# Performance work log

Measured on AMD Instinct MI355X. Metric: run time of the kernel, lower is better.

## Reference

```python
import jax, jax.numpy as jnp
import numpy as np

NUM_NODES_GLOBAL = 100000
EMBED_DIM = 256
NUM_RELATIONS = 16
N_LOCAL = 16384
N_EDGES = 131072
N_QUERIES = 4096


def setup_inputs() -> dict:
    key = jax.random.key(0)
    ks = jax.random.split(key, 12)
    node_emb = jax.random.normal(ks[0], (NUM_NODES_GLOBAL, EMBED_DIM), dtype=jnp.float32)
    # RGCN layer 1 params: per-relation weight (R, in, out), root weight, bias
    w1 = jax.random.normal(ks[1], (NUM_RELATIONS, EMBED_DIM, EMBED_DIM), dtype=jnp.float32) * 0.05
    root1 = jax.random.normal(ks[2], (EMBED_DIM, EMBED_DIM), dtype=jnp.float32) * 0.05
    b1 = jnp.zeros((EMBED_DIM,), dtype=jnp.float32)
    w2 = jax.random.normal(ks[3], (NUM_RELATIONS, EMBED_DIM, EMBED_DIM), dtype=jnp.float32) * 0.05
    root2 = jax.random.normal(ks[4], (EMBED_DIM, EMBED_DIM), dtype=jnp.float32) * 0.05
    b2 = jnp.zeros((EMBED_DIM,), dtype=jnp.float32)
    edge_index = jax.random.randint(ks[5], (2, N_EDGES), 0, N_LOCAL, dtype=jnp.int64)
    edge_type = jax.random.randint(ks[6], (N_EDGES,), 0, NUM_RELATIONS, dtype=jnp.int64)
    entity_ids = jax.random.randint(ks[7], (N_LOCAL,), 0, NUM_NODES_GLOBAL, dtype=jnp.int64)
    batch_ids = jnp.sort(jax.random.randint(ks[8], (N_LOCAL,), 0, N_QUERIES, dtype=jnp.int64))
    return {"node_emb": node_emb, "w1": w1, "root1": root1, "b1": b1,
            "w2": w2, "root2": root2, "b2": b2,
            "edge_index": edge_index, "edge_type": edge_type,
            "entity_ids": entity_ids, "batch_ids": batch_ids}


def rgcn_layer(x, W, Wroot, b, src, tgt, edge_type, num_relations):
    """PyG RGCNConv (num_bases=None, aggr='mean', root_weight=True, bias=True).

    out[i] = sum_r mean_{j: (j -r-> i)} x_j @ W[r]  +  x_i @ Wroot + b
    Aggregation done per (target, relation) bucket, then a single (N,R,d)x(R,d,d) einsum.
    """
    n = x.shape[0]
    d = x.shape[1]
    bucket = tgt * num_relations + edge_type  # (E,) combined (node, relation) key
    ones = jnp.ones(src.shape, dtype=x.dtype)
    cnt = jax.ops.segment_sum(ones, bucket, num_segments=n * num_relations)
    agg = jax.ops.segment_sum(x[src], bucket, num_segments=n * num_relations)
    agg = agg.reshape(n, num_relations, d) / jnp.maximum(cnt, 1.0).reshape(n, num_relations, 1)
    return jnp.einsum('nrd,rdo->no', agg, W) + x @ Wroot + b


def reference(node_emb, w1, root1, b1, w2, root2, b2, edge_index, edge_type, entity_ids, batch_ids):
    x = node_emb[entity_ids]                      # (N_local, d) gather from global table
    src, tgt = edge_index[0], edge_index[1]
    x = rgcn_layer(x, w1, root1, b1, src, tgt, edge_type, NUM_RELATIONS)
    x = rgcn_layer(x, w2, root2, b2, src, tgt, edge_type, NUM_RELATIONS)
    # scatter-sum readout per query
    return jax.ops.segment_sum(x, batch_ids, num_segments=N_QUERIES)
```

## Files before the change

kernel.cpp:

```cpp
#include <hip/hip_runtime.h>
#include <hip/hip_bf16.h>

#define NLOCAL 16384
#define NEDGES 131072
#define NREL   16
#define DIM    256
#define NQ     4096
#define NBLKS  512

typedef __bf16 bf16x8 __attribute__((ext_vector_type(8)));
typedef float  f32x4  __attribute__((ext_vector_type(4)));
typedef unsigned short u16x8 __attribute__((ext_vector_type(8)));

static __device__ __forceinline__ unsigned short f2bf(float f) {
    union { float f; unsigned u; } v; v.f = f;
    unsigned r = v.u + 0x7FFFu + ((v.u >> 16) & 1u);
    return (unsigned short)(r >> 16);
}
static __device__ __forceinline__ float bf2f(unsigned short s) {
    union { unsigned u; float f; } v; v.u = ((unsigned)s) << 16;
    return v.f;
}

__global__ void k_gather(const float* __restrict__ emb, const int* __restrict__ ids,
                         unsigned short* __restrict__ x0) {
    int gid = blockIdx.x * blockDim.x + threadIdx.x;
    int i = gid >> 5, c8 = gid & 31;
    int e = ids[i];
    const f32x4* src = (const f32x4*)(emb + (size_t)e * DIM + c8 * 8);
    f32x4 a = src[0], b = src[1];
    u16x8 u;
    u[0] = f2bf(a[0]); u[1] = f2bf(a[1]); u[2] = f2bf(a[2]); u[3] = f2bf(a[3]);
    u[4] = f2bf(b[0]); u[5] = f2bf(b[1]); u[6] = f2bf(b[2]); u[7] = f2bf(b[3]);
    *(u16x8*)&x0[(size_t)i * DIM + c8 * 8] = u;
}

__global__ void k_transpose_all(const float* __restrict__ w1, const float* __restrict__ r1,
                                const float* __restrict__ w2, const float* __restrict__ r2,
                                unsigned short* __restrict__ WT1, unsigned short* __restrict__ rT1,
                                unsigned short* __restrict__ WT2, unsigned short* __restrict__ rT2) {
    __shared__ float t[64][65];
    int blk = blockIdx.x;
    const float* W; unsigned short* WT; int tr;
    if (blk < 256)      { W = w1 + (size_t)(blk >> 4) * DIM * DIM; WT = WT1 + (size_t)(blk >> 4) * DIM * DIM; tr = blk & 15; }
    else if (blk < 272) { W = r1; WT = rT1; tr = blk - 256; }
    else if (blk < 528) { int q = blk - 272; W = w2 + (size_t)(q >> 4) * DIM * DIM; WT = WT2 + (size_t)(q >> 4) * DIM * DIM; tr = q & 15; }
    else                { W = r2; WT = rT2; tr = blk - 528; }
    int tk = (tr >> 2) << 6;
    int to = (tr & 3) << 6;
    #pragma unroll
    for (int it = 0; it < 16; ++it) {
        int el = it * 256 + threadIdx.x;
        int row = el >> 6, col = el & 63;
        t[row][col] = W[(size_t)(tk + row) * DIM + to + col];
    }
    __syncthreads();
    #pragma unroll
    for (int it = 0; it < 16; ++it) {
        int el = it * 256 + threadIdx.x;
        int row = el >> 6, col = el & 63;
        WT[(size_t)(to + row) * DIM + tk + col] = f2bf(t[col][row]);
    }
}

__global__ void k_hist2(const int* __restrict__ eidx, const int* __restrict__ etype,
                        unsigned int* __restrict__ cnt, int* __restrict__ bh) {
    __shared__ int h[NREL];
    int tid = threadIdx.x;
    if (tid < NREL) h[tid] = 0;
    __syncthreads();
    int e = blockIdx.x * 256 + tid;
    int rel = etype[e];
    int tgt = eidx[NEDGES + e];
    atomicAdd(&cnt[tgt * NREL + rel], 1u);
    atomicAdd(&h[rel], 1);
    __syncthreads();
    if (tid < NREL) bh[tid * NBLKS + blockIdx.x] = h[tid];
}

__global__ void k_scan_par(int* __restrict__ bh, int* __restrict__ meta) {
    __shared__ int tot[NREL];
    __shared__ int base[NREL];
    int w = threadIdx.x >> 6, lane = threadIdx.x & 63;
    int vals[8];
    int run = 0;
    #pragma unroll
    for (int c = 0; c < 8; ++c) {
        int v = bh[w * NBLKS + c * 64 + lane];
        int s = v;
        #pragma unroll
        for (int off = 1; off < 64; off <<= 1) {
            int t = __shfl_up(s, off);
            if (lane >= off) s += t;
        }
        vals[c] = run + s - v;
        run += __shfl(s, 63);
    }
    if (lane == 0) tot[w] = run;
    __syncthreads();
    if (threadIdx.x == 0) {
        int s = 0;
        for (int r = 0; r < NREL; ++r) { base[r] = s; meta[16 + r] = s; s += (tot[r] + 63) & ~63; }
        meta[32] = s;
    }
    __syncthreads();
    int b = base[w];
    #pragma unroll
    for (int c = 0; c < 8; ++c) bh[w * NBLKS + c * 64 + lane] = vals[c] + b;
}

__global__ void k_place2(const int* __restrict__ eidx, const int* __restrict__ etype,
                         const int* __restrict__ bh, int* __restrict__ ssrc,
                         int* __restrict__ stgt) {
    __shared__ int cur[NREL];
    int tid = threadIdx.x;
    if (tid < NREL) cur[tid] = bh[tid * NBLKS + blockIdx.x];
    __syncthreads();
    int e = blockIdx.x * 256 + tid;
    int rel = etype[e];
    int pos = atomicAdd(&cur[rel], 1);
    ssrc[pos] = eidx[e];
    stgt[pos] = eidx[NEDGES + e];
}

#define AS_IDX(row, c16) ((row) * 64 + (((c16) ^ ((row) & 7)) << 3))

__launch_bounds__(256)
__global__ void k_gemm_root(const unsigned short* __restrict__ X, const unsigned short* __restrict__ BT,
                            const float* __restrict__ bias, unsigned short* __restrict__ Y) {
    __shared__ __align__(16) unsigned short As[64 * 64];
    __shared__ __align__(16) unsigned short Bs[256 * 64];
    int tid = threadIdx.x;
    int wave = tid >> 6, lane = tid & 63;
    int l16 = lane & 15, grp = lane >> 4;
    int bm = blockIdx.x;

    f32x4 acc[4][4];
    #pragma unroll
    for (int i = 0; i < 4; ++i)
        #pragma unroll
        for (int j = 0; j < 4; ++j) acc[i][j] = f32x4{0.f, 0.f, 0.f, 0.f};

    int arow = tid >> 3, ac16 = tid & 7;
    for (int kt = 0; kt < 4; ++kt) {
        #pragma unroll
        for (int it = 0; it < 2; ++it) {
            int row = it * 32 + arow;
            u16x8 u = *(const u16x8*)&X[(size_t)(bm * 64 + row) * DIM + kt * 64 + ac16 * 8];
            *(u16x8*)&As[AS_IDX(row, ac16)] = u;
        }
        #pragma unroll
        for (int it = 0; it < 8; ++it) {
            int flat = it * 256 + tid;
            int row = flat >> 3, c16 = flat & 7;
            u16x8 u = *(const u16x8*)&BT[(size_t)row * DIM + kt * 64 + c16 * 8];
            *(u16x8*)&Bs[AS_IDX(row, c16)] = u;
        }
        __syncthreads();
        #pragma unroll
        for (int kk = 0; kk < 2; ++kk) {
            bf16x8 a[4], b[4];
            #pragma unroll
            for (int i = 0; i < 4; ++i) {
                int row = i * 16 + l16;
                a[i] = *(const bf16x8*)&As[AS_IDX(row, kk * 4 + grp)];
            }
            #pragma unroll
            for (int j = 0; j < 4; ++j) {
                int row = wave * 64 + j * 16 + l16;
                b[j] = *(const bf16x8*)&Bs[AS_IDX(row, kk * 4 + grp)];
            }
            #pragma unroll
            for (int i = 0; i < 4; ++i)
                #pragma unroll
                for (int j = 0; j < 4; ++j)
                    acc[i][j] = __builtin_amdgcn_mfma_f32_16x16x32_bf16(a[i], b[j], acc[i][j], 0, 0, 0);
        }
        __syncthreads();
    }
    #pragma unroll
    for (int i = 0; i < 4; ++i)
        #pragma unroll
        for (int reg = 0; reg < 4; ++reg) {
            int row = i * 16 + grp * 4 + reg;
            int gr = bm * 64 + row;
            #pragma unroll
            for (int j = 0; j < 4; ++j) {
                int col = wave * 64 + j * 16 + l16;
                float v = acc[i][j][reg] + bias[col];
                float vo = __shfl_xor(v, 1);
                if (!(lane & 1)) {
                    unsigned pk = (unsigned)f2bf(v) | ((unsigned)f2bf(vo) << 16);
                    *(unsigned*)&Y[(size_t)gr * DIM + col] = pk;
                }
            }
        }
}

__launch_bounds__(256)
__global__ void k_gemm_edge(const unsigned short* __restrict__ X, const unsigned short* __restrict__ WT,
                            const int* __restrict__ ssrc, const int* __restrict__ stgt,
                            const unsigned int* __restrict__ cnt, const int* __restrict__ meta,
                            unsigned short* __restrict__ Y) {
    int base = blockIdx.x * 64;
    if (base >= meta[32]) return;
    int rel = 0;
    while (rel < 15 && meta[16 + rel + 1] <= base) ++rel;
    const unsigned short* BT = WT + (size_t)rel * DIM * DIM;

    __shared__ __align__(16) unsigned short As[64 * 64];
    __shared__ __align__(16) unsigned short Bs[256 * 64];
    int tid = threadIdx.x;
    int wave = tid >> 6, lane = tid & 63;
    int l16 = lane & 15, grp = lane >> 4;

    f32x4 acc[4][4];
    #pragma unroll
    for (int i = 0; i < 4; ++i)
        #pragma unroll
        for (int j = 0; j < 4; ++j) acc[i][j] = f32x4{0.f, 0.f, 0.f, 0.f};

    int arow = tid >> 3, ac16 = tid & 7;
    int s0 = ssrc[base + arow];
    int s1 = ssrc[base + 32 + arow];
    for (int kt = 0; kt < 4; ++kt) {
        #pragma unroll
        for (int it = 0; it < 2; ++it) {
            int row = it * 32 + arow;
            int s = it ? s1 : s0;
            u16x8 u = {};
            if (s >= 0) u = *(const u16x8*)&X[(size_t)s * DIM + kt * 64 + ac16 * 8];
            *(u16x8*)&As[AS_IDX(row, ac16)] = u;
        }
        #pragma unroll
        for (int it = 0; it < 8; ++it) {
            int flat = it * 256 + tid;
            int row = flat >> 3, c16 = flat & 7;
            u16x8 u = *(const u16x8*)&BT[(size_t)row * DIM + kt * 64 + c16 * 8];
            *(u16x8*)&Bs[AS_IDX(row, c16)] = u;
        }
        __syncthreads();
        #pragma unroll
        for (int kk = 0; kk < 2; ++kk) {
            bf16x8 a[4], b[4];
            #pragma unroll
            for (int i = 0; i < 4; ++i) {
                int row = i * 16 + l16;
                a[i] = *(const bf16x8*)&As[AS_IDX(row, kk * 4 + grp)];
            }
            #pragma unroll
            for (int j = 0; j < 4; ++j) {
                int row = wave * 64 + j * 16 + l16;
                b[j] = *(const bf16x8*)&Bs[AS_IDX(row, kk * 4 + grp)];
            }
            #pragma unroll
            for (int i = 0; i < 4; ++i)
                #pragma unroll
                for (int j = 0; j < 4; ++j)
                    acc[i][j] = __builtin_amdgcn_mfma_f32_16x16x32_bf16(a[i], b[j], acc[i][j], 0, 0, 0);
        }
        __syncthreads();
    }
    #pragma unroll
    for (int i = 0; i < 4; ++i)
        #pragma unroll
        for (int reg = 0; reg < 4; ++reg) {
            int row = i * 16 + grp * 4 + reg;
            int e = base + row;
            int s = ssrc[e];
            if (s < 0) continue;
            int tgt = stgt[e];
            float rc = 1.0f / fmaxf((float)cnt[tgt * NREL + rel], 1.0f);
            unsigned short* Yrow = Y + (size_t)tgt * DIM;
            #pragma unroll
            for (int j = 0; j < 4; ++j) {
                int col = wave * 64 + j * 16 + l16;
                float v = acc[i][j][reg] * rc;
                float vo = __shfl_xor(v, 1);
                if (!(lane & 1)) {
                    __hip_bfloat162 hv;
                    ((unsigned short*)&hv)[0] = f2bf(v);
                    ((unsigned short*)&hv)[1] = f2bf(vo);
                    unsafeAtomicAdd((__hip_bfloat162*)(Yrow + col), hv);
                }
            }
        }
}

__global__ void k_readout(const unsigned short* __restrict__ X2, const int* __restrict__ bids,
                          float* __restrict__ out) {
    int gid = blockIdx.x * blockDim.x + threadIdx.x;
    int g = gid >> 5, c8 = gid & 31;
    int i0 = g * 8;
    float a[8];
    #pragma unroll
    for (int j = 0; j < 8; ++j) a[j] = 0.f;
    int curq = bids[i0];
    #pragma unroll
    for (int t = 0; t < 8; ++t) {
        int i = i0 + t;
        int q = bids[i];
        if (q != curq) {
            #pragma unroll
            for (int j = 0; j < 8; ++j) {
                unsafeAtomicAdd(&out[(size_t)curq * DIM + c8 * 8 + j], a[j]);
                a[j] = 0.f;
            }
            curq = q;
        }
        u16x8 v = *(const u16x8*)&X2[(size_t)i * DIM + c8 * 8];
        #pragma unroll
        for (int j = 0; j < 8; ++j) a[j] += bf2f(v[j]);
    }
    #pragma unroll
    for (int j = 0; j < 8; ++j)
        unsafeAtomicAdd(&out[(size_t)curq * DIM + c8 * 8 + j], a[j]);
}

extern "C" void kernel_launch(void* const* d_in, const int* in_sizes, int n_in,
                              void* d_out, int out_size, void* d_ws, size_t ws_size,
                              hipStream_t stream) {
    const float* emb   = (const float*)d_in[0];
    const float* w1    = (const float*)d_in[1];
    const float* root1 = (const float*)d_in[2];
    const float* b1    = (const float*)d_in[3];
    const float* w2    = (const float*)d_in[4];
    const float* root2 = (const float*)d_in[5];
    const float* b2    = (const float*)d_in[6];
    const int* eidx    = (const int*)d_in[7];
    const int* etype   = (const int*)d_in[8];
    const int* eids    = (const int*)d_in[9];
    const int* bids    = (const int*)d_in[10];
    float* out = (float*)d_out;

    char* ws = (char*)d_ws;
    unsigned short* x0  = (unsigned short*)(ws + (size_t)(0 << 20));
    unsigned short* x1  = (unsigned short*)(ws + (size_t)(8 << 20));
    unsigned short* x2  = (unsigned short*)(ws + (size_t)(16 << 20));
    unsigned short* WT1 = (unsigned short*)(ws + (size_t)(24 << 20));
    unsigned short* rT1 = (unsigned short*)(ws + (size_t)(26 << 20));
    unsigned short* WT2 = (unsigned short*)(ws + (size_t)(27 << 20));
    unsigned short* rT2 = (unsigned short*)(ws + (size_t)(29 << 20));
    unsigned int*   cnt = (unsigned int*)(ws + (size_t)(30 << 20));
    int*           meta = (int*)(ws + (size_t)(31 << 20));
    int*           ssrc = (int*)(ws + (size_t)(31 << 20) + 4096);
    int*           stgt = (int*)(ws + (size_t)(32 << 20));
    int*           bh   = (int*)(ws + (size_t)(33 << 20));

    const int NBLK_EDGE = (NEDGES + NREL * 64) / 64;

    hipMemsetAsync(cnt, 0, (size_t)NLOCAL * NREL * 4, stream);
    hipMemsetAsync(ssrc, 0xFF, (size_t)(NEDGES + NREL * 64) * 4, stream);
    hipMemsetAsync(out, 0, (size_t)NQ * DIM * 4, stream);

    k_gather<<<2048, 256, 0, stream>>>(emb, eids, x0);
    k_transpose_all<<<544, 256, 0, stream>>>(w1, root1, w2, root2, WT1, rT1, WT2, rT2);
    k_hist2<<<NBLKS, 256, 0, stream>>>(eidx, etype, cnt, bh);
    k_scan_par<<<1, 1024, 0, stream>>>(bh, meta);
    k_place2<<<NBLKS, 256, 0, stream>>>(eidx, etype, bh, ssrc, stgt);

    k_gemm_root<<<NLOCAL / 64, 256, 0, stream>>>(x0, rT1, b1, x1);
    k_gemm_edge<<<NBLK_EDGE, 256, 0, stream>>>(x0, WT1, ssrc, stgt, cnt, meta, x1);
    k_gemm_root<<<NLOCAL / 64, 256, 0, stream>>>(x1, rT2, b2, x2);
    k_gemm_edge<<<NBLK_EDGE, 256, 0, stream>>>(x1, WT2, ssrc, stgt, cnt, meta, x2);

    k_readout<<<256, 256, 0, stream>>>(x2, bids, out);
}
```

Before: 505.6 us.

## Replace bf16 atomic scatter with per-edge buffer and CSR gather-combine

The edge GEMM now writes each scaled edge message to a per-slot buffer instead of doing bf16x2 atomic adds into the target rows. A per-target CSR (count, scan, placement) is built, and a new combine kernel sums the root output plus all incoming edge messages per target in fp32. The GEMMs also drop LDS staging of the weight tile, reading B fragments directly from global/L2, and double-buffer the A tile with one sync per k-step. This trades atomic contention and repeated bf16 rounding for extra memory traffic (a 64MB-class edge buffer written and re-read) plus two extra setup kernels.

```diff
diff --git a/kernel.cpp b/kernel.cpp
--- a/kernel.cpp
+++ b/kernel.cpp
@@ -7,9 +7,11 @@
 #define DIM    256
 #define NQ     4096
 #define NBLKS  512
+#define NSLOTS (NEDGES + NREL * 64)
 
 typedef __bf16 bf16x8 __attribute__((ext_vector_type(8)));
 typedef float  f32x4  __attribute__((ext_vector_type(4)));
+typedef unsigned short u16x4 __attribute__((ext_vector_type(4)));
 typedef unsigned short u16x8 __attribute__((ext_vector_type(8)));
 
 static __device__ __forceinline__ unsigned short f2bf(float f) {
@@ -64,7 +66,8 @@
 }
 
 __global__ void k_hist2(const int* __restrict__ eidx, const int* __restrict__ etype,
-                        unsigned int* __restrict__ cnt, int* __restrict__ bh) {
+                        unsigned int* __restrict__ cnt, unsigned int* __restrict__ cnt_t,
+                        int* __restrict__ bh) {
     __shared__ int h[NREL];
     int tid = threadIdx.x;
     if (tid < NREL) h[tid] = 0;
@@ -73,6 +76,7 @@
     int rel = etype[e];
     int tgt = eidx[NEDGES + e];
     atomicAdd(&cnt[tgt * NREL + rel], 1u);
+    atomicAdd(&cnt_t[tgt], 1u);
     atomicAdd(&h[rel], 1);
     __syncthreads();
     if (tid < NREL) bh[tid * NBLKS + blockIdx.x] = h[tid];
@@ -123,17 +127,57 @@
     stgt[pos] = eidx[NEDGES + e];
 }
 
+__global__ void k_scan_t(const unsigned int* __restrict__ cnt_t, int* __restrict__ row_ptr,
+                         int* __restrict__ cur) {
+    __shared__ int wsum[16];
+    int tid = threadIdx.x;
+    int wave = tid >> 6, lane = tid & 63;
+    int base = tid * 16;
+    int loc[16];
+    int s = 0;
+    #pragma unroll
+    for (int c = 0; c < 16; ++c) { loc[c] = s; s += (int)cnt_t[base + c]; }
+    int inc = s;
+    #pragma unroll
+    for (int off = 1; off < 64; off <<= 1) {
+        int t = __shfl_up(inc, off);
+        if (lane >= off) inc += t;
+    }
+    if (lane == 63) wsum[wave] = inc;
+    __syncthreads();
+    if (tid == 0) {
+        int a = 0;
+        for (int w = 0; w < 16; ++w) { int v = wsum[w]; wsum[w] = a; a += v; }
+    }
+    __syncthreads();
+    int excl = wsum[wave] + inc - s;
+    #pragma unroll
+    for (int c = 0; c < 16; ++c) { int v = excl + loc[c]; row_ptr[base + c] = v; cur[base + c] = v; }
+    if (tid == 1023) row_ptr[NLOCAL] = excl + s;
+}
+
+__global__ void k_place_t(const int* __restrict__ ssrc, const int* __restrict__ stgt,
+                          int* __restrict__ cur, int* __restrict__ elist) {
+    int p = blockIdx.x * 256 + threadIdx.x;
+    int s = ssrc[p];
+    if (s >= 0) {
+        int tgt = stgt[p];
+        int pos = atomicAdd(&cur[tgt], 1);
+        elist[pos] = p;
+    }
+}
+
 #define AS_IDX(row, c16) ((row) * 64 + (((c16) ^ ((row) & 7)) << 3))
 
 __launch_bounds__(256)
 __global__ void k_gemm_root(const unsigned short* __restrict__ X, const unsigned short* __restrict__ BT,
                             const float* __restrict__ bias, unsigned short* __restrict__ Y) {
-    __shared__ __align__(16) unsigned short As[64 * 64];
-    __shared__ __align__(16) unsigned short Bs[256 * 64];
+    __shared__ __align__(16) unsigned short As[2][64 * 64];
     int tid = threadIdx.x;
     int wave = tid >> 6, lane = tid & 63;
     int l16 = lane & 15, grp = lane >> 4;
     int bm = blockIdx.x;
+    int arow = tid >> 3, ac16 = tid & 7;
 
     f32x4 acc[4][4];
     #pragma unroll
@@ -141,42 +185,38 @@
         #pragma unroll
         for (int j = 0; j < 4; ++j) acc[i][j] = f32x4{0.f, 0.f, 0.f, 0.f};
 
-    int arow = tid >> 3, ac16 = tid & 7;
+    #pragma unroll
+    for (int it = 0; it < 2; ++it) {
+        int row = it * 32 + arow;
+        u16x8 u = *(const u16x8*)&X[(size_t)(bm * 64 + row) * DIM + ac16 * 8];
+        *(u16x8*)&As[0][AS_IDX(row, ac16)] = u;
+    }
     for (int kt = 0; kt < 4; ++kt) {
-        #pragma unroll
-        for (int it = 0; it < 2; ++it) {
-            int row = it * 32 + arow;
-            u16x8 u = *(const u16x8*)&X[(size_t)(bm * 64 + row) * DIM + kt * 64 + ac16 * 8];
-            *(u16x8*)&As[AS_IDX(row, ac16)] = u;
-        }
-        #pragma unroll
-        for (int it = 0; it < 8; ++it) {
-            int flat = it * 256 + tid;
-            int row = flat >> 3, c16 = flat & 7;
-            u16x8 u = *(const u16x8*)&BT[(size_t)row * DIM + kt * 64 + c16 * 8];
-            *(u16x8*)&Bs[AS_IDX(row, c16)] = u;
-        }
         __syncthreads();
+        if (kt < 3) {
+            #pragma unroll
+            for (int it = 0; it < 2; ++it) {
+                int row = it * 32 + arow;
+                u16x8 u = *(const u16x8*)&X[(size_t)(bm * 64 + row) * DIM + (kt + 1) * 64 + ac16 * 8];
+                *(u16x8*)&As[(kt + 1) & 1][AS_IDX(row, ac16)] = u;
+            }
+        }
+        const unsigned short* buf = As[kt & 1];
         #pragma unroll
         for (int kk = 0; kk < 2; ++kk) {
             bf16x8 a[4], b[4];
             #pragma unroll
-            for (int i = 0; i < 4; ++i) {
-                int row = i * 16 + l16;
-                a[i] = *(const bf16x8*)&As[AS_IDX(row, kk * 4 + grp)];
-            }
-            #pragma unroll
-            for (int j = 0; j < 4; ++j) {
-                int row = wave * 64 + j * 16 + l16;
-                b[j] = *(const bf16x8*)&Bs[AS_IDX(row, kk * 4 + grp)];
-            }
+            for (int i = 0; i < 4; ++i)
+                a[i] = *(const bf16x8*)&buf[AS_IDX(i * 16 + l16, kk * 4 + grp)];
+            #pragma unroll
+            for (int j = 0; j < 4; ++j)
+                b[j] = *(const bf16x8*)&BT[(size_t)(wave * 64 + j * 16 + l16) * DIM + kt * 64 + kk * 32 + grp * 8];
             #pragma unroll
             for (int i = 0; i < 4; ++i)
                 #pragma unroll
                 for (int j = 0; j < 4; ++j)
                     acc[i][j] = __builtin_amdgcn_mfma_f32_16x16x32_bf16(a[i], b[j], acc[i][j], 0, 0, 0);
         }
-        __syncthreads();
     }
     #pragma unroll
     for (int i = 0; i < 4; ++i)
@@ -201,18 +241,18 @@
 __global__ void k_gemm_edge(const unsigned short* __restrict__ X, const unsigned short* __restrict__ WT,
                             const int* __restrict__ ssrc, const int* __restrict__ stgt,
                             const unsigned int* __restrict__ cnt, const int* __restrict__ meta,
-                            unsigned short* __restrict__ Y) {
+                            unsigned short* __restrict__ ye) {
     int base = blockIdx.x * 64;
     if (base >= meta[32]) return;
     int rel = 0;
     while (rel < 15 && meta[16 + rel + 1] <= base) ++rel;
     const unsigned short* BT = WT + (size_t)rel * DIM * DIM;
 
-    __shared__ __align__(16) unsigned short As[64 * 64];
-    __shared__ __align__(16) unsigned short Bs[256 * 64];
+    __shared__ __align__(16) unsigned short As[2][64 * 64];
     int tid = threadIdx.x;
     int wave = tid >> 6, lane = tid & 63;
     int l16 = lane & 15, grp = lane >> 4;
+    int arow = tid >> 3, ac16 = tid & 7;
 
     f32x4 acc[4][4];
     #pragma unroll
@@ -220,46 +260,44 @@
         #pragma unroll
         for (int j = 0; j < 4; ++j) acc[i][j] = f32x4{0.f, 0.f, 0.f, 0.f};
 
-    int arow = tid >> 3, ac16 = tid & 7;
     int s0 = ssrc[base + arow];
     int s1 = ssrc[base + 32 + arow];
+    #pragma unroll
+    for (int it = 0; it < 2; ++it) {
+        int row = it * 32 + arow;
+        int s = it ? s1 : s0;
+        u16x8 u = {};
+        if (s >= 0) u = *(const u16x8*)&X[(size_t)s * DIM + ac16 * 8];
+        *(u16x8*)&As[0][AS_IDX(row, ac16)] = u;
+    }
     for (int kt = 0; kt < 4; ++kt) {
-        #pragma unroll
-        for (int it = 0; it < 2; ++it) {
-            int row = it * 32 + arow;
-            int s = it ? s1 : s0;
-            u16x8 u = {};
-            if (s >= 0) u = *(const u16x8*)&X[(size_t)s * DIM + kt * 64 + ac16 * 8];
-            *(u16x8*)&As[AS_IDX(row, ac16)] = u;
-        }
-        #pragma unroll
-        for (int it = 0; it < 8; ++it) {
-            int flat = it * 256 + tid;
-            int row = flat >> 3, c16 = flat & 7;
-            u16x8 u = *(const u16x8*)&BT[(size_t)row * DIM + kt * 64 + c16 * 8];
-            *(u16x8*)&Bs[AS_IDX(row, c16)] = u;
-        }
         __syncthreads();
+        if (kt < 3) {
+            #pragma unroll
+            for (int it = 0; it < 2; ++it) {
+                int row = it * 32 + arow;
+                int s = it ? s1 : s0;
+                u16x8 u = {};
+                if (s >= 0) u = *(const u16x8*)&X[(size_t)s * DIM + (kt + 1) * 64 + ac16 * 8];
+                *(u16x8*)&As[(kt + 1) & 1][AS_IDX(row, ac16)] = u;
+            }
+        }
+        const unsigned short* buf = As[kt & 1];
         #pragma unroll
         for (int kk = 0; kk < 2; ++kk) {
             bf16x8 a[4], b[4];
             #pragma unroll
-            for (int i = 0; i < 4; ++i) {
-                int row = i * 16 + l16;
-                a[i] = *(const bf16x8*)&As[AS_IDX(row, kk * 4 + grp)];
-            }
-            #pragma unroll
-            for (int j = 0; j < 4; ++j) {
-                int row = wave * 64 + j * 16 + l16;
-                b[j] = *(const bf16x8*)&Bs[AS_IDX(row, kk * 4 + grp)];
-            }
+            for (int i = 0; i < 4; ++i)
+                a[i] = *(const bf16x8*)&buf[AS_IDX(i * 16 + l16, kk * 4 + grp)];
+            #pragma unroll
+            for (int j = 0; j < 4; ++j)
+                b[j] = *(const bf16x8*)&BT[(size_t)(wave * 64 + j * 16 + l16) * DIM + kt * 64 + kk * 32 + grp * 8];
             #pragma unroll
             for (int i = 0; i < 4; ++i)
                 #pragma unroll
                 for (int j = 0; j < 4; ++j)
                     acc[i][j] = __builtin_amdgcn_mfma_f32_16x16x32_bf16(a[i], b[j], acc[i][j], 0, 0, 0);
         }
-        __syncthreads();
     }
     #pragma unroll
     for (int i = 0; i < 4; ++i)
@@ -268,23 +306,38 @@
             int row = i * 16 + grp * 4 + reg;
             int e = base + row;
             int s = ssrc[e];
-            if (s < 0) continue;
             int tgt = stgt[e];
-            float rc = 1.0f / fmaxf((float)cnt[tgt * NREL + rel], 1.0f);
-            unsigned short* Yrow = Y + (size_t)tgt * DIM;
+            float rc = (s >= 0) ? 1.0f / fmaxf((float)cnt[tgt * NREL + rel], 1.0f) : 0.0f;
             #pragma unroll
             for (int j = 0; j < 4; ++j) {
                 int col = wave * 64 + j * 16 + l16;
                 float v = acc[i][j][reg] * rc;
                 float vo = __shfl_xor(v, 1);
-                if (!(lane & 1)) {
-                    __hip_bfloat162 hv;
-                    ((unsigned short*)&hv)[0] = f2bf(v);
-                    ((unsigned short*)&hv)[1] = f2bf(vo);
-                    unsafeAtomicAdd((__hip_bfloat162*)(Yrow + col), hv);
+                if (s >= 0 && !(lane & 1)) {
+                    unsigned pk = (unsigned)f2bf(v) | ((unsigned)f2bf(vo) << 16);
+                    *(unsigned*)&ye[(size_t)e * DIM + col] = pk;
                 }
             }
         }
+}
+
+__global__ void k_combine(const unsigned short* __restrict__ rootY, const unsigned short* __restrict__ ye,
+                          const int* __restrict__ row_ptr, const int* __restrict__ elist,
+                          unsigned short* __restrict__ Xout) {
+    int wave = threadIdx.x >> 6, lane = threadIdx.x & 63;
+    int tgt = blockIdx.x * 4 + wave;
+    int c0 = lane * 4;
+    u16x4 rv = *(const u16x4*)&rootY[(size_t)tgt * DIM + c0];
+    float a0 = bf2f(rv[0]), a1 = bf2f(rv[1]), a2 = bf2f(rv[2]), a3 = bf2f(rv[3]);
+    int p0 = row_ptr[tgt], p1 = row_ptr[tgt + 1];
+    for (int p = p0; p < p1; ++p) {
+        int idx = elist[p];
+        u16x4 v = *(const u16x4*)&ye[(size_t)idx * DIM + c0];
+        a0 += bf2f(v[0]); a1 += bf2f(v[1]); a2 += bf2f(v[2]); a3 += bf2f(v[3]);
+    }
+    u16x4 o;
+    o[0] = f2bf(a0); o[1] = f2bf(a1); o[2] = f2bf(a2); o[3] = f2bf(a3);
+    *(u16x4*)&Xout[(size_t)tgt * DIM + c0] = o;
 }
 
 __global__ void k_readout(const unsigned short* __restrict__ X2, const int* __restrict__ bids,
@@ -334,35 +387,46 @@
     float* out = (float*)d_out;
 
     char* ws = (char*)d_ws;
-    unsigned short* x0  = (unsigned short*)(ws + (size_t)(0 << 20));
-    unsigned short* x1  = (unsigned short*)(ws + (size_t)(8 << 20));
-    unsigned short* x2  = (unsigned short*)(ws + (size_t)(16 << 20));
-    unsigned short* WT1 = (unsigned short*)(ws + (size_t)(24 << 20));
-    unsigned short* rT1 = (unsigned short*)(ws + (size_t)(26 << 20));
-    unsigned short* WT2 = (unsigned short*)(ws + (size_t)(27 << 20));
-    unsigned short* rT2 = (unsigned short*)(ws + (size_t)(29 << 20));
-    unsigned int*   cnt = (unsigned int*)(ws + (size_t)(30 << 20));
-    int*           meta = (int*)(ws + (size_t)(31 << 20));
-    int*           ssrc = (int*)(ws + (size_t)(31 << 20) + 4096);
-    int*           stgt = (int*)(ws + (size_t)(32 << 20));
-    int*           bh   = (int*)(ws + (size_t)(33 << 20));
-
-    const int NBLK_EDGE = (NEDGES + NREL * 64) / 64;
+    unsigned short* x0   = (unsigned short*)(ws + (size_t)(0 << 20));
+    unsigned short* x1   = (unsigned short*)(ws + (size_t)(8 << 20));
+    unsigned short* x2   = (unsigned short*)(ws + (size_t)(16 << 20));
+    unsigned short* WT1  = (unsigned short*)(ws + (size_t)(24 << 20));
+    unsigned short* rT1  = (unsigned short*)(ws + (size_t)(26 << 20));
+    unsigned short* WT2  = (unsigned short*)(ws + (size_t)(27 << 20));
+    unsigned short* rT2  = (unsigned short*)(ws + (size_t)(29 << 20));
+    unsigned int*   cnt  = (unsigned int*)(ws + (size_t)(30 << 20));
+    int*           meta  = (int*)(ws + (size_t)(31 << 20));
+    int*           ssrc  = (int*)(ws + (size_t)(31 << 20) + 4096);
+    int*           stgt  = (int*)(ws + (size_t)(32 << 20));
+    int*           bh    = (int*)(ws + (size_t)(33 << 20));
+    unsigned int*  cnt_t = (unsigned int*)(ws + (size_t)(33 << 20) + 65536);
+    int*         row_ptr = (int*)(ws + (size_t)(33 << 20) + 2 * 65536);
+    int*           cur_t = (int*)(ws + (size_t)(33 << 20) + 3 * 65536 + 4096);
+    int*           elist = (int*)(ws + (size_t)(34 << 20));
+    unsigned short* rootY= (unsigned short*)(ws + (size_t)(35 << 20));
+    unsigned short* ye   = (unsigned short*)(ws + (size_t)(43 << 20));
+
+    const int NBLK_EDGE = NSLOTS / 64;
 
     hipMemsetAsync(cnt, 0, (size_t)NLOCAL * NREL * 4, stream);
-    hipMemsetAsync(ssrc, 0xFF, (size_t)(NEDGES + NREL * 64) * 4, stream);
+    hipMemsetAsync(cnt_t, 0, (size_t)NLOCAL * 4, stream);
+    hipMemsetAsync(ssrc, 0xFF, (size_t)NSLOTS * 4, stream);
     hipMemsetAsync(out, 0, (size_t)NQ * DIM * 4, stream);
 
     k_gather<<<2048, 256, 0, stream>>>(emb, eids, x0);
     k_transpose_all<<<544, 256, 0, stream>>>(w1, root1, w2, root2, WT1, rT1, WT2, rT2);
-    k_hist2<<<NBLKS, 256, 0, stream>>>(eidx, etype, cnt, bh);
+    k_hist2<<<NBLKS, 256, 0, stream>>>(eidx, etype, cnt, cnt_t, bh);
     k_scan_par<<<1, 1024, 0, stream>>>(bh, meta);
     k_place2<<<NBLKS, 256, 0, stream>>>(eidx, etype, bh, ssrc, stgt);
-
-    k_gemm_root<<<NLOCAL / 64, 256, 0, stream>>>(x0, rT1, b1, x1);
-    k_gemm_edge<<<NBLK_EDGE, 256, 0, stream>>>(x0, WT1, ssrc, stgt, cnt, meta, x1);
-    k_gemm_root<<<NLOCAL / 64, 256, 0, stream>>>(x1, rT2, b2, x2);
-    k_gemm_edge<<<NBLK_EDGE, 256, 0, stream>>>(x1, WT2, ssrc, stgt, cnt, meta, x2);
+    k_scan_t<<<1, 1024, 0, stream>>>(cnt_t, row_ptr, cur_t);
+    k_place_t<<<NSLOTS / 256, 256, 0, stream>>>(ssrc, stgt, cur_t, elist);
+
+    k_gemm_root<<<NLOCAL / 64, 256, 0, stream>>>(x0, rT1, b1, rootY);
+    k_gemm_edge<<<NBLK_EDGE, 256, 0, stream>>>(x0, WT1, ssrc, stgt, cnt, meta, ye);
+    k_combine<<<NLOCAL / 4, 256, 0, stream>>>(rootY, ye, row_ptr, elist, x1);
+    k_gemm_root<<<NLOCAL / 64, 256, 0, stream>>>(x1, rT2, b2, rootY);
+    k_gemm_edge<<<NBLK_EDGE, 256, 0, stream>>>(x1, WT2, ssrc, stgt, cnt, meta, ye);
+    k_combine<<<NLOCAL / 4, 256, 0, stream>>>(rootY, ye, row_ptr, elist, x2);
 
     k_readout<<<256, 256, 0, stream>>>(x2, bids, out);
 }
```

After: 470.2 us. 1.08x faster.
